# Kernel optimization log

Hardware: AMD Instinct MI355X
Metric: run time of the kernel (lower is better)

## Reference

```python
import jax, jax.numpy as jnp
import numpy as np
from jax import lax

V = 50000      # node_num
LN = 128       # feat_dim
S = 16         # stat_dim
E = 500000     # n_edges
T = 3          # propagation steps
MU = 0.9


def setup_inputs() -> dict:
    key = jax.random.key(0)
    ks = jax.random.split(key, 10)
    X_Node = jax.random.randint(ks[0], (E,), 0, V, dtype=jnp.int32)
    X_Neis = jax.random.randint(ks[1], (E,), 0, V, dtype=jnp.int32)
    dg_list = jax.random.randint(ks[2], (E,), 1, 64, dtype=jnp.int32)
    emb = jax.random.normal(ks[3], (V, LN), dtype=jnp.float32) * 0.1
    xi_w = jax.random.normal(ks[4], (2 * LN, S * S), dtype=jnp.float32) * (1.0 / np.sqrt(2 * LN))
    xi_b = jnp.zeros((S * S,), dtype=jnp.float32)
    rou_w = jax.random.normal(ks[5], (LN, S), dtype=jnp.float32) * (1.0 / np.sqrt(LN))
    rou_b = jnp.zeros((S,), dtype=jnp.float32)
    lin_w = jax.random.normal(ks[6], (LN + S, 3), dtype=jnp.float32) * (1.0 / np.sqrt(LN + S))
    lin_b = jnp.zeros((3,), dtype=jnp.float32)
    return {"X_Node": X_Node, "X_Neis": X_Neis, "dg_list": dg_list,
            "emb": emb, "xi_w": xi_w, "xi_b": xi_b,
            "rou_w": rou_w, "rou_b": rou_b, "lin_w": lin_w, "lin_b": lin_b}


def reference(X_Node, X_Neis, dg_list, emb, xi_w, xi_b, rou_w, rou_b, lin_w, lin_b):
    # edge features: concat(src embed, nbr embed) -> [E, 2*ln]
    Xn = emb[X_Node]                                  # [E, ln]
    X = jnp.concatenate([Xn, emb[X_Neis]], axis=1)    # [E, 2*ln]
    dg = dg_list.astype(emb.dtype)
    # Hw: A = Xi(X)*mu/s/dg  (constant across iterations; torch recomputes, same math)
    A = jnp.tanh(X @ xi_w + xi_b).reshape(-1, S, S)   # [E, s, s]
    A = A * (MU / S) / dg[:, None, None]
    b = jnp.tanh(Xn @ rou_w + rou_b)                  # [E, s]

    states0 = jnp.zeros((V, S), dtype=emb.dtype)

    def step(states, _):
        H = states[X_Node]                            # [E, s] gather
        H = jnp.einsum('est,et->es', A, H) + b        # per-edge small matvec
        states = jax.ops.segment_sum(H, X_Neis, num_segments=V)  # scatter-sum (AggrSum)
        return states, None

    states, _ = lax.scan(step, states0, None, length=T)
    logits = jnp.concatenate([emb, states], axis=1) @ lin_w + lin_b  # [V, 3]
    return jax.nn.softmax(logits, axis=1)
```

## Files before the change

### kernel.cpp

```cpp
#include <hip/hip_runtime.h>
#include <hip/hip_bf16.h>
#include <hip/hip_fp16.h>

#define LN_F 128

typedef __attribute__((ext_vector_type(8))) __bf16 bf16x8;
typedef __attribute__((ext_vector_type(4))) float f32x4;
typedef __attribute__((ext_vector_type(2))) _Float16 half2_t;

__device__ __forceinline__ unsigned short f2bf(float f) {
    unsigned u = __float_as_uint(f);
    u = u + 0x7FFFu + ((u >> 16) & 1u);
    return (unsigned short)(u >> 16);
}
__device__ __forceinline__ float tanh_polyc(float x) {
    x = fminf(1.2f, fmaxf(-1.2f, x));
    float t = x * x;
    float p = fmaf(t, -0.05396825397f, 0.13333333333f);
    p = fmaf(t, p, -0.33333333333f);
    p = fmaf(t, p, 1.0f);
    return x * p;
}
__device__ __forceinline__ float bflo(unsigned u) { return __uint_as_float(u << 16); }
__device__ __forceinline__ float bfhi(unsigned u) { return __uint_as_float(u & 0xffff0000u); }

__device__ __forceinline__ unsigned f2e5(float x) {
    unsigned short u = __half_as_ushort(__float2half(x));
    u = (unsigned short)(u + 0x7F + ((u >> 8) & 1));
    return (unsigned)(u >> 8) & 0xFFu;
}
__device__ __forceinline__ half2_t u2h2(unsigned w) {
    union { unsigned u; half2_t h; } c; c.u = w; return c.h;
}
__device__ __forceinline__ unsigned h2u(half2_t h) {
    union { half2_t h; unsigned u; } c; c.h = h; return c.u;
}
__device__ __forceinline__ half2_t tanh_pk(half2_t x) {
    const half2_t c2 = {(_Float16)(2.0f / 15.0f), (_Float16)(2.0f / 15.0f)};
    const half2_t c1 = {(_Float16)(-1.0f / 3.0f), (_Float16)(-1.0f / 3.0f)};
    const half2_t one = {(_Float16)1.0f, (_Float16)1.0f};
    half2_t t = x * x;
    half2_t p = t * c2 + c1;
    p = t * p + one;
    return x * p;
}

__global__ void k_conv(const float* __restrict__ emb, const float* __restrict__ xiw,
                       const float* __restrict__ rw,
                       unsigned short* __restrict__ embb, unsigned short* __restrict__ WcT,
                       unsigned short* __restrict__ rouT, int V) {
    int t = blockIdx.x * blockDim.x + threadIdx.x;
    int n_emb = V * 16;
    if (t < n_emb) {
        const float4* s = (const float4*)emb;
        float4 a = s[t * 2], b = s[t * 2 + 1];
        uint4 o;
        o.x = (unsigned)f2bf(a.x) | ((unsigned)f2bf(a.y) << 16);
        o.y = (unsigned)f2bf(a.z) | ((unsigned)f2bf(a.w) << 16);
        o.z = (unsigned)f2bf(b.x) | ((unsigned)f2bf(b.y) << 16);
        o.w = (unsigned)f2bf(b.z) | ((unsigned)f2bf(b.w) << 16);
        ((uint4*)embb)[t] = o;
    } else if (t < n_emb + 512 * 16) {
        int t2 = t - n_emb;
        int cp = t2 >> 4, g = t2 & 15;
        unsigned short u[8];
#pragma unroll
        for (int j = 0; j < 8; ++j) {
            int k = g * 8 + j;
            float w = (cp < 256) ? xiw[k * 256 + cp] : xiw[(128 + k) * 256 + (cp - 256)];
            u[j] = f2bf(w);
        }
        uint4 o;
        o.x = (unsigned)u[0] | ((unsigned)u[1] << 16);
        o.y = (unsigned)u[2] | ((unsigned)u[3] << 16);
        o.z = (unsigned)u[4] | ((unsigned)u[5] << 16);
        o.w = (unsigned)u[6] | ((unsigned)u[7] << 16);
        ((uint4*)WcT)[cp * 16 + (g ^ (cp & 7))] = o;
    } else if (t < n_emb + 512 * 16 + 256) {
        int t2 = t - n_emb - 512 * 16;
        int c = t2 >> 4, g = t2 & 15;
        unsigned short u[8];
#pragma unroll
        for (int j = 0; j < 8; ++j) u[j] = f2bf(rw[(g * 8 + j) * 16 + c]);
        uint4 o;
        o.x = (unsigned)u[0] | ((unsigned)u[1] << 16);
        o.y = (unsigned)u[2] | ((unsigned)u[3] << 16);
        o.z = (unsigned)u[4] | ((unsigned)u[5] << 16);
        o.w = (unsigned)u[6] | ((unsigned)u[7] << 16);
        ((uint4*)rouT)[c * 16 + (g ^ (c & 7))] = o;
    }
}

__global__ void k_hist(const int* __restrict__ Xe, int* __restrict__ cnt, int n) {
    int e = blockIdx.x * blockDim.x + threadIdx.x;
    if (e < n) atomicAdd(&cnt[Xe[e]], 1);
}

__global__ __launch_bounds__(256) void k_scan1(const int* __restrict__ cnt,
                                               int* __restrict__ rp,
                                               int* __restrict__ bsum, int V) {
    __shared__ int ls[256];
    int b = blockIdx.x, t = threadIdx.x;
    int i = b * 256 + t;
    int val = (i < V) ? cnt[i] : 0;
    ls[t] = val;
    __syncthreads();
    for (int off = 1; off < 256; off <<= 1) {
        int x = (t >= off) ? ls[t - off] : 0;
        __syncthreads();
        ls[t] += x;
        __syncthreads();
    }
    if (i < V) rp[i] = ls[t] - val;
    if (t == 255) bsum[b] = ls[255];
}

__global__ __launch_bounds__(256) void k_scan2(const int* __restrict__ bsum,
                                               int* __restrict__ boff,
                                               int* __restrict__ rp, int V, int NB) {
    __shared__ int ls[256];
    int t = threadIdx.x;
    int val = (t < NB) ? bsum[t] : 0;
    ls[t] = val;
    __syncthreads();
    for (int off = 1; off < 256; off <<= 1) {
        int x = (t >= off) ? ls[t - off] : 0;
        __syncthreads();
        ls[t] += x;
        __syncthreads();
    }
    if (t < NB) boff[t] = ls[t] - val;
    if (t == 255) rp[V] = ls[255];
}

__global__ void k_scan3(int* __restrict__ rp, const int* __restrict__ boff, int V) {
    int i = blockIdx.x * blockDim.x + threadIdx.x;
    if (i < V) rp[i] += boff[blockIdx.x];
}

__global__ void k_permute(const int* __restrict__ Xn, const int* __restrict__ Xe,
                          const int* __restrict__ dg, const int* __restrict__ rp,
                          int* __restrict__ c2, int2* __restrict__ edata,
                          int* __restrict__ edst, int n) {
    int e = blockIdx.x * blockDim.x + threadIdx.x;
    if (e >= n) return;
    int nb = Xe[e];
    int pos = rp[nb] + atomicAdd(&c2[nb], 1);
    edata[pos] = make_int2(Xn[e], __float_as_int(0.05625f / (float)dg[e]));
    edst[pos] = nb;
}

__global__ void k_padfill(int2* __restrict__ edata, int* __restrict__ edst,
                          int E, int Epad) {
    int i = E + blockIdx.x * blockDim.x + threadIdx.x;
    if (i >= Epad) return;
    edata[i] = make_int2(0, 0);
    edst[i] = 0;
}

__global__ __launch_bounds__(512) void k_U(
    const unsigned short* __restrict__ embb, const uint4* __restrict__ WcT,
    const uint4* __restrict__ rouT, const float* __restrict__ xib,
    const float* __restrict__ roub,
    unsigned* __restrict__ U8, unsigned* __restrict__ U28,
    float* __restrict__ bnode, int V) {
    __shared__ uint4 sB[2048];
    __shared__ uint4 sR[256];
    const int half = blockIdx.y;
    for (int i = threadIdx.x; i < 2048; i += 512) sB[i] = WcT[half * 2048 + i];
    if (half == 0 && threadIdx.x < 256) sR[threadIdx.x] = rouT[threadIdx.x];
    __syncthreads();

    const int wave = threadIdx.x >> 6, lane = threadIdx.x & 63;
    const int j = lane & 15, kg = lane >> 4;
    const int wbase = blockIdx.x * 512 + wave * 64;

    int nv[4];
#pragma unroll
    for (int g = 0; g < 4; ++g) nv[g] = min(wbase + g * 16 + j, V - 1);

    f32x4 acc[8][4] = {};
    f32x4 accb[4] = {};
#pragma unroll
    for (int kc = 0; kc < 4; ++kc) {
        bf16x8 bf[4];
#pragma unroll
        for (int g = 0; g < 4; ++g)
            bf[g] = *(const bf16x8*)(embb + (size_t)nv[g] * 128 + kc * 32 + kg * 8);
        int swz = (kc * 4 + kg) ^ (j & 7);
#pragma unroll
        for (int ct = 0; ct < 8; ++ct) {
            bf16x8 afr = ((const bf16x8*)sB)[(ct * 16 + j) * 16 + swz];
#pragma unroll
            for (int g = 0; g < 4; ++g)
                acc[ct][g] = __builtin_amdgcn_mfma_f32_16x16x32_bf16(afr, bf[g], acc[ct][g], 0, 0, 0);
        }
        if (half == 0) {
            bf16x8 rfr = ((const bf16x8*)sR)[j * 16 + swz];
#pragma unroll
            for (int g = 0; g < 4; ++g)
                accb[g] = __builtin_amdgcn_mfma_f32_16x16x32_bf16(rfr, bf[g], accb[g], 0, 0, 0);
        }
    }

#pragma unroll
    for (int ct = 0; ct < 8; ++ct) {
        int c0 = half * 128 + ct * 16 + kg * 4;
        float4 bias = (half < 2) ? ((const float4*)xib)[c0 >> 2]
                                 : make_float4(0.f, 0.f, 0.f, 0.f);
#pragma unroll
        for (int g = 0; g < 4; ++g) {
            int node = wbase + g * 16 + j;
            if (node < V) {
                const f32x4 a = acc[ct][g];
                float v0 = a[0] + bias.x, v1 = a[1] + bias.y;
                float v2 = a[2] + bias.z, v3 = a[3] + bias.w;
                unsigned pk = f2e5(v0) | (f2e5(v1) << 8) | (f2e5(v2) << 16) | (f2e5(v3) << 24);
                if (half < 2) U8[node * 64 + (c0 >> 2)] = pk;
                else          U28[node * 64 + ((c0 - 256) >> 2)] = pk;
            }
        }
    }
    if (half == 0) {
        float4 rb4 = ((const float4*)roub)[kg];
#pragma unroll
        for (int g = 0; g < 4; ++g) {
            int node = wbase + g * 16 + j;
            if (node < V) {
                float4 bo;
                bo.x = tanh_polyc(accb[g][0] + rb4.x);
                bo.y = tanh_polyc(accb[g][1] + rb4.y);
                bo.z = tanh_polyc(accb[g][2] + rb4.z);
                bo.w = tanh_polyc(accb[g][3] + rb4.w);
                *(float4*)(bnode + (size_t)node * 16 + kg * 4) = bo;
            }
        }
    }
}

__global__ __launch_bounds__(256) void k_B1e(
    const float* __restrict__ bnode, const int2* __restrict__ edata,
    const int* __restrict__ edst, float* __restrict__ B1, int E, int Epad) {
    int wid = (blockIdx.x * 256 + threadIdx.x) >> 6;
    int wbase = wid * 64;
    if (wbase >= Epad) return;
    int lane = threadIdx.x & 63;
    int g = lane >> 4, s = lane & 15, lbase = g * 16;
    int sbase = wbase + g * 16;

    int em = wbase + lane;
    int d_own = edst[em];
    int d_nxt = edst[min(em + 1, Epad - 1)];
    unsigned long long flags = __ballot(d_own != d_nxt);

    int cur = edst[sbase];
    float acc = 0.f;
#pragma unroll 4
    for (int j = 0; j < 16; ++j) {
        int p = sbase + j;
        int u = edata[p].x;
        float v = bnode[(size_t)u * 16 + s];
        acc += (p < E) ? v : 0.f;
        bool flush = ((flags >> (lbase + j)) & 1ull) || (j == 15);
        if (flush) {
            atomicAdd(&B1[(size_t)cur * 16 + s], acc);
            acc = 0.f;
            if (j < 15) cur = edst[p + 1];
        }
    }
}

__global__ void k_prep(const float* __restrict__ st, unsigned* __restrict__ Hf,
                       float* __restrict__ cp1, float* __restrict__ cp2, int n2) {
    int i = blockIdx.x * blockDim.x + threadIdx.x;
    if (i >= n2) return;
    float2 f = ((const float2*)st)[i];
    half2_t h = {(_Float16)f.x, (_Float16)f.y};
    Hf[i] = h2u(h);
    if (cp1 != nullptr) {
        ((float2*)cp1)[i] = f;
        ((float2*)cp2)[i] = f;
    }
}

__global__ __launch_bounds__(256) void k_prop_e(
    const unsigned* __restrict__ U8, const unsigned* __restrict__ U28,
    const int2* __restrict__ edata, const int* __restrict__ edst,
    const unsigned* __restrict__ Hf,
    float* __restrict__ sn, int Epad) {
    int wid = (blockIdx.x * 256 + threadIdx.x) >> 6;
    int wbase = wid * 64;
    if (wbase >= Epad) return;
    int lane = threadIdx.x & 63;
    int g = lane >> 4, s = lane & 15, lbase = g * 16;
    int sbase = wbase + g * 16;

    int em = wbase + lane;
    int d_own = edst[em];
    int d_nxt = edst[min(em + 1, Epad - 1)];
    unsigned long long flags = __ballot(d_own != d_nxt);

    int cur = edst[sbase];
    half2_t u2h[8];
    {
        uint4 r = ((const uint4*)U28)[cur * 16 + s];
        unsigned wr[4] = {r.x, r.y, r.z, r.w};
#pragma unroll
        for (int q = 0; q < 4; ++q) {
            u2h[2 * q]     = u2h2(__builtin_amdgcn_perm(wr[q], 0u, 0x05000400u));
            u2h[2 * q + 1] = u2h2(__builtin_amdgcn_perm(wr[q], 0u, 0x07000600u));
        }
    }

    float acc = 0.f;
#pragma unroll 2
    for (int j = 0; j < 16; ++j) {
        int p = sbase + j;
        int2 ed = edata[p];
        int u = ed.x;
        float sc = __int_as_float(ed.y);
        uint4 q1 = ((const uint4*)U8)[u * 16 + s];
        unsigned h2 = Hf[u * 8 + (s & 7)];
        unsigned wq[4] = {q1.x, q1.y, q1.z, q1.w};
        float sum = 0.f;
#pragma unroll
        for (int q = 0; q < 4; ++q) {
            half2_t x0 = u2h2(__builtin_amdgcn_perm(wq[q], 0u, 0x05000400u)) + u2h[2 * q];
            half2_t x1 = u2h2(__builtin_amdgcn_perm(wq[q], 0u, 0x07000600u)) + u2h[2 * q + 1];
            half2_t r0 = tanh_pk(x0);
            half2_t r1 = tanh_pk(x1);
            unsigned hm0 = __shfl(h2, lbase + 2 * q, 64);
            unsigned hm1 = __shfl(h2, lbase + 2 * q + 1, 64);
            sum = __builtin_amdgcn_fdot2(r0, u2h2(hm0), sum, false);
            sum = __builtin_amdgcn_fdot2(r1, u2h2(hm1), sum, false);
        }
        acc = fmaf(sc, sum, acc);
        bool flush = ((flags >> (lbase + j)) & 1ull) || (j == 15);
        if (flush) {
            atomicAdd(&sn[(size_t)cur * 16 + s], acc);
            acc = 0.f;
            if (j < 15) {
                cur = edst[p + 1];
                uint4 r = ((const uint4*)U28)[cur * 16 + s];
                unsigned wr[4] = {r.x, r.y, r.z, r.w};
#pragma unroll
                for (int q = 0; q < 4; ++q) {
                    u2h[2 * q]     = u2h2(__builtin_amdgcn_perm(wr[q], 0u, 0x05000400u));
                    u2h[2 * q + 1] = u2h2(__builtin_amdgcn_perm(wr[q], 0u, 0x07000600u));
                }
            }
        }
    }
}

__global__ void k_final(const unsigned short* __restrict__ embb, const float* __restrict__ st,
                        const float* __restrict__ lw, const float* __restrict__ lb,
                        float* __restrict__ out, int nv) {
    __shared__ float sw[435];
    for (int i = threadIdx.x; i < 435; i += 256) sw[i] = (i < 432) ? lw[i] : lb[i - 432];
    __syncthreads();
    int t = blockIdx.x * blockDim.x + threadIdx.x;
    int v = t >> 4, j = t & 15;
    if (v >= nv) return;
    const uint4 q = *(const uint4*)(embb + (size_t)v * 128 + j * 8);
    unsigned uu[4] = {q.x, q.y, q.z, q.w};
    float a0 = 0.f, a1 = 0.f, a2 = 0.f;
#pragma unroll
    for (int m = 0; m < 4; ++m) {
        int i = j * 8 + 2 * m;
        float x0 = bflo(uu[m]), x1 = bfhi(uu[m]);
        a0 += x0 * sw[i * 3] + x1 * sw[(i + 1) * 3];
        a1 += x0 * sw[i * 3 + 1] + x1 * sw[(i + 1) * 3 + 1];
        a2 += x0 * sw[i * 3 + 2] + x1 * sw[(i + 1) * 3 + 2];
    }
    float xs = st[(size_t)v * 16 + j];
    a0 += xs * sw[(128 + j) * 3]; a1 += xs * sw[(128 + j) * 3 + 1]; a2 += xs * sw[(128 + j) * 3 + 2];
#pragma unroll
    for (int m = 1; m < 16; m <<= 1) {
        a0 += __shfl_xor(a0, m, 64);
        a1 += __shfl_xor(a1, m, 64);
        a2 += __shfl_xor(a2, m, 64);
    }
    if (j == 0) {
        a0 += sw[432]; a1 += sw[433]; a2 += sw[434];
        float mx = fmaxf(a0, fmaxf(a1, a2));
        float e0 = __expf(a0 - mx), e1 = __expf(a1 - mx), e2 = __expf(a2 - mx);
        float inv = 1.f / (e0 + e1 + e2);
        out[(size_t)v * 3 + 0] = e0 * inv;
        out[(size_t)v * 3 + 1] = e1 * inv;
        out[(size_t)v * 3 + 2] = e2 * inv;
    }
}

extern "C" void kernel_launch(void* const* d_in, const int* in_sizes, int n_in,
                              void* d_out, int out_size, void* d_ws, size_t ws_size,
                              hipStream_t stream) {
    const int*   Xn  = (const int*)d_in[0];
    const int*   Xe  = (const int*)d_in[1];
    const int*   dg  = (const int*)d_in[2];
    const float* emb = (const float*)d_in[3];
    const float* xiw = (const float*)d_in[4];
    const float* xib = (const float*)d_in[5];
    const float* rw  = (const float*)d_in[6];
    const float* rb  = (const float*)d_in[7];
    const float* lw  = (const float*)d_in[8];
    const float* lb  = (const float*)d_in[9];
    float* out = (float*)d_out;
    const int E = in_sizes[0];
    const int V = in_sizes[3] / LN_F;
    const int NB = (V + 255) / 256;
    const int Epad = (E + 63) & ~63;

    char* p = (char*)d_ws;
    auto carve = [&](size_t bytes) {
        char* q = p; p += (bytes + 255) & ~(size_t)255; return q;
    };
    unsigned short* embb = (unsigned short*)carve((size_t)V * 128 * 2);
    unsigned* U8    = (unsigned*)carve((size_t)V * 256);
    unsigned* U28   = (unsigned*)carve((size_t)V * 256);
    uint4* WcT   = (uint4*)carve(512 * 16 * 16);
    uint4* rouT  = (uint4*)carve(4096);
    float* bnode = (float*)carve((size_t)V * 16 * 4);
    float* B1    = (float*)carve((size_t)V * 16 * 4);
    float* stB   = (float*)carve((size_t)V * 16 * 4);
    float* stA   = (float*)carve((size_t)V * 16 * 4);
    unsigned* Hf = (unsigned*)carve((size_t)V * 16 * 2);
    int*   cnt   = (int*)carve((size_t)V * 4 * 2);
    int*   c2    = cnt + V;
    int*   rp    = (int*)carve((size_t)(V + 1) * 4);
    int*   bsum  = (int*)carve(256 * 4);
    int*   boff  = (int*)carve(256 * 4);
    int2*  edata = (int2*)carve((size_t)Epad * 8);
    int*   edst  = (int*)carve((size_t)Epad * 4);

    {
        int nconv = V * 16 + 512 * 16 + 256;
        k_conv<<<(nconv + 255) / 256, 256, 0, stream>>>(
            emb, xiw, rw, embb, (unsigned short*)WcT, (unsigned short*)rouT, V);
        dim3 g((V + 511) / 512, 4);
        k_U<<<g, 512, 0, stream>>>(embb, WcT, rouT, xib, rb, U8, U28, bnode, V);
    }

    hipMemsetAsync(cnt, 0, (size_t)V * 4 * 2, stream);
    k_hist<<<(E + 255) / 256, 256, 0, stream>>>(Xe, cnt, E);
    k_scan1<<<NB, 256, 0, stream>>>(cnt, rp, bsum, V);
    k_scan2<<<1, 256, 0, stream>>>(bsum, boff, rp, V, NB);
    k_scan3<<<NB, 256, 0, stream>>>(rp, boff, V);
    k_permute<<<(E + 255) / 256, 256, 0, stream>>>(Xn, Xe, dg, rp, c2, edata, edst, E);
    if (Epad > E)
        k_padfill<<<1, 64, 0, stream>>>(edata, edst, E, Epad);

    hipMemsetAsync(B1, 0, (size_t)V * 16 * 4, stream);
    {
        int blocks = (Epad / 64 + 3) / 4;
        k_B1e<<<blocks, 256, 0, stream>>>(bnode, edata, edst, B1, E, Epad);
    }

    const int n2 = V * 8;
    const int pblocks = (Epad / 64 + 3) / 4;

    k_prep<<<(n2 + 255) / 256, 256, 0, stream>>>(B1, Hf, stB, stA, n2);
    k_prop_e<<<pblocks, 256, 0, stream>>>(U8, U28, edata, edst, Hf, stB, Epad);

    k_prep<<<(n2 + 255) / 256, 256, 0, stream>>>(stB, Hf, nullptr, nullptr, n2);
    k_prop_e<<<pblocks, 256, 0, stream>>>(U8, U28, edata, edst, Hf, stA, Epad);

    k_final<<<((size_t)V * 16 + 255) / 256, 256, 0, stream>>>(embb, stA, lw, lb, out, V);
}
```

Measured before the change: 201.8 us.

## Fuse histogram and B1 zeroing into conversion kernel; shuffle edge data across lanes

Merges the destination histogram and the B1 zero-fill into the bf16 conversion kernel, folds the pad fill into the permute kernel, and zeroes both counter arrays with a single memset. This cuts kernel launches and memsets. In the edge kernels, each lane now loads its own edata and edst entry once, and the inner loops read them with wave shuffles instead of repeated global loads. The unroll factor of the propagation loop rises from 2 to 4. The extra shuffles add instruction overhead, and the larger unroll may raise register pressure.

```diff
diff --git a/kernel.cpp b/kernel.cpp
--- a/kernel.cpp
+++ b/kernel.cpp
@@ -46,9 +46,10 @@
 }
 
 __global__ void k_conv(const float* __restrict__ emb, const float* __restrict__ xiw,
-                       const float* __restrict__ rw,
+                       const float* __restrict__ rw, const int* __restrict__ Xe,
                        unsigned short* __restrict__ embb, unsigned short* __restrict__ WcT,
-                       unsigned short* __restrict__ rouT, int V) {
+                       unsigned short* __restrict__ rouT, int* __restrict__ cnt,
+                       float* __restrict__ B1, int V, int E) {
     int t = blockIdx.x * blockDim.x + threadIdx.x;
     int n_emb = V * 16;
     if (t < n_emb) {
@@ -60,6 +61,7 @@
         o.z = (unsigned)f2bf(b.x) | ((unsigned)f2bf(b.y) << 16);
         o.w = (unsigned)f2bf(b.z) | ((unsigned)f2bf(b.w) << 16);
         ((uint4*)embb)[t] = o;
+        B1[t] = 0.f;
     } else if (t < n_emb + 512 * 16) {
         int t2 = t - n_emb;
         int cp = t2 >> 4, g = t2 & 15;
@@ -89,11 +91,7 @@
         o.w = (unsigned)u[6] | ((unsigned)u[7] << 16);
         ((uint4*)rouT)[c * 16 + (g ^ (c & 7))] = o;
     }
-}
-
-__global__ void k_hist(const int* __restrict__ Xe, int* __restrict__ cnt, int n) {
-    int e = blockIdx.x * blockDim.x + threadIdx.x;
-    if (e < n) atomicAdd(&cnt[Xe[e]], 1);
+    if (t < E) atomicAdd(&cnt[Xe[t]], 1);
 }
 
 __global__ __launch_bounds__(256) void k_scan1(const int* __restrict__ cnt,
@@ -141,21 +139,17 @@
 __global__ void k_permute(const int* __restrict__ Xn, const int* __restrict__ Xe,
                           const int* __restrict__ dg, const int* __restrict__ rp,
                           int* __restrict__ c2, int2* __restrict__ edata,
-                          int* __restrict__ edst, int n) {
+                          int* __restrict__ edst, int n, int Epad) {
     int e = blockIdx.x * blockDim.x + threadIdx.x;
-    if (e >= n) return;
-    int nb = Xe[e];
-    int pos = rp[nb] + atomicAdd(&c2[nb], 1);
-    edata[pos] = make_int2(Xn[e], __float_as_int(0.05625f / (float)dg[e]));
-    edst[pos] = nb;
-}
-
-__global__ void k_padfill(int2* __restrict__ edata, int* __restrict__ edst,
-                          int E, int Epad) {
-    int i = E + blockIdx.x * blockDim.x + threadIdx.x;
-    if (i >= Epad) return;
-    edata[i] = make_int2(0, 0);
-    edst[i] = 0;
+    if (e < n) {
+        int nb = Xe[e];
+        int pos = rp[nb] + atomicAdd(&c2[nb], 1);
+        edata[pos] = make_int2(Xn[e], __float_as_int(0.05625f / (float)dg[e]));
+        edst[pos] = nb;
+    } else if (e < Epad) {
+        edata[e] = make_int2(0, 0);
+        edst[e] = 0;
+    }
 }
 
 __global__ __launch_bounds__(512) void k_U(
@@ -246,26 +240,27 @@
     if (wbase >= Epad) return;
     int lane = threadIdx.x & 63;
     int g = lane >> 4, s = lane & 15, lbase = g * 16;
-    int sbase = wbase + g * 16;
+    int sbase = wbase + lbase;
 
     int em = wbase + lane;
+    int my_u = edata[em].x;
     int d_own = edst[em];
     int d_nxt = edst[min(em + 1, Epad - 1)];
     unsigned long long flags = __ballot(d_own != d_nxt);
 
-    int cur = edst[sbase];
+    int cur = __shfl(d_own, lbase, 64);
     float acc = 0.f;
 #pragma unroll 4
     for (int j = 0; j < 16; ++j) {
         int p = sbase + j;
-        int u = edata[p].x;
+        int u = __shfl(my_u, lbase + j, 64);
         float v = bnode[(size_t)u * 16 + s];
         acc += (p < E) ? v : 0.f;
         bool flush = ((flags >> (lbase + j)) & 1ull) || (j == 15);
         if (flush) {
             atomicAdd(&B1[(size_t)cur * 16 + s], acc);
             acc = 0.f;
-            if (j < 15) cur = edst[p + 1];
+            if (j < 15) cur = __shfl(d_nxt, lbase + j, 64);
         }
     }
 }
@@ -293,14 +288,14 @@
     if (wbase >= Epad) return;
     int lane = threadIdx.x & 63;
     int g = lane >> 4, s = lane & 15, lbase = g * 16;
-    int sbase = wbase + g * 16;
 
     int em = wbase + lane;
+    int2 myed = edata[em];
     int d_own = edst[em];
     int d_nxt = edst[min(em + 1, Epad - 1)];
     unsigned long long flags = __ballot(d_own != d_nxt);
 
-    int cur = edst[sbase];
+    int cur = __shfl(d_own, lbase, 64);
     half2_t u2h[8];
     {
         uint4 r = ((const uint4*)U28)[cur * 16 + s];
@@ -313,12 +308,10 @@
     }
 
     float acc = 0.f;
-#pragma unroll 2
+#pragma unroll 4
     for (int j = 0; j < 16; ++j) {
-        int p = sbase + j;
-        int2 ed = edata[p];
-        int u = ed.x;
-        float sc = __int_as_float(ed.y);
+        int u = __shfl(myed.x, lbase + j, 64);
+        float sc = __int_as_float(__shfl(myed.y, lbase + j, 64));
         uint4 q1 = ((const uint4*)U8)[u * 16 + s];
         unsigned h2 = Hf[u * 8 + (s & 7)];
         unsigned wq[4] = {q1.x, q1.y, q1.z, q1.w};
@@ -340,7 +333,7 @@
             atomicAdd(&sn[(size_t)cur * 16 + s], acc);
             acc = 0.f;
             if (j < 15) {
-                cur = edst[p + 1];
+                cur = __shfl(d_nxt, lbase + j, 64);
                 uint4 r = ((const uint4*)U28)[cur * 16 + s];
                 unsigned wr[4] = {r.x, r.y, r.z, r.w};
 #pragma unroll
@@ -415,50 +408,54 @@
     auto carve = [&](size_t bytes) {
         char* q = p; p += (bytes + 255) & ~(size_t)255; return q;
     };
+    int*   cnt   = (int*)carve((size_t)V * 4);
+    int*   c2    = (int*)carve((size_t)V * 4);
+    size_t zero_bytes = (size_t)(p - (char*)cnt);
+    float* B1    = (float*)carve((size_t)V * 16 * 4);
     unsigned short* embb = (unsigned short*)carve((size_t)V * 128 * 2);
     unsigned* U8    = (unsigned*)carve((size_t)V * 256);
     unsigned* U28   = (unsigned*)carve((size_t)V * 256);
     uint4* WcT   = (uint4*)carve(512 * 16 * 16);
     uint4* rouT  = (uint4*)carve(4096);
     float* bnode = (float*)carve((size_t)V * 16 * 4);
-    float* B1    = (float*)carve((size_t)V * 16 * 4);
     float* stB   = (float*)carve((size_t)V * 16 * 4);
     float* stA   = (float*)carve((size_t)V * 16 * 4);
     unsigned* Hf = (unsigned*)carve((size_t)V * 16 * 2);
-    int*   cnt   = (int*)carve((size_t)V * 4 * 2);
-    int*   c2    = cnt + V;
     int*   rp    = (int*)carve((size_t)(V + 1) * 4);
     int*   bsum  = (int*)carve(256 * 4);
     int*   boff  = (int*)carve(256 * 4);
     int2*  edata = (int2*)carve((size_t)Epad * 8);
     int*   edst  = (int*)carve((size_t)Epad * 4);
 
+    hipMemsetAsync(cnt, 0, zero_bytes, stream);
+
     {
         int nconv = V * 16 + 512 * 16 + 256;
-        k_conv<<<(nconv + 255) / 256, 256, 0, stream>>>(
-            emb, xiw, rw, embb, (unsigned short*)WcT, (unsigned short*)rouT, V);
-        dim3 g((V + 511) / 512, 4);
-        k_U<<<g, 512, 0, stream>>>(embb, WcT, rouT, xib, rb, U8, U28, bnode, V);
-    }
-
-    hipMemsetAsync(cnt, 0, (size_t)V * 4 * 2, stream);
-    k_hist<<<(E + 255) / 256, 256, 0, stream>>>(Xe, cnt, E);
+        int ntot = nconv > E ? nconv : E;
+        k_conv<<<(ntot + 255) / 256, 256, 0, stream>>>(
+            emb, xiw, rw, Xe, embb, (unsigned short*)WcT, (unsigned short*)rouT,
+            cnt, B1, V, E);
+    }
+
     k_scan1<<<NB, 256, 0, stream>>>(cnt, rp, bsum, V);
     k_scan2<<<1, 256, 0, stream>>>(bsum, boff, rp, V, NB);
     k_scan3<<<NB, 256, 0, stream>>>(rp, boff, V);
-    k_permute<<<(E + 255) / 256, 256, 0, stream>>>(Xn, Xe, dg, rp, c2, edata, edst, E);
-    if (Epad > E)
-        k_padfill<<<1, 64, 0, stream>>>(edata, edst, E, Epad);
-
-    hipMemsetAsync(B1, 0, (size_t)V * 16 * 4, stream);
+
     {
-        int blocks = (Epad / 64 + 3) / 4;
-        k_B1e<<<blocks, 256, 0, stream>>>(bnode, edata, edst, B1, E, Epad);
+        int ng = (Epad > E ? Epad : E);
+        k_permute<<<(ng + 255) / 256, 256, 0, stream>>>(Xn, Xe, dg, rp, c2, edata, edst, E, Epad);
+    }
+
+    {
+        dim3 g((V + 511) / 512, 4);
+        k_U<<<g, 512, 0, stream>>>(embb, WcT, rouT, xib, rb, U8, U28, bnode, V);
     }
 
     const int n2 = V * 8;
     const int pblocks = (Epad / 64 + 3) / 4;
 
+    k_B1e<<<pblocks, 256, 0, stream>>>(bnode, edata, edst, B1, E, Epad);
+
     k_prep<<<(n2 + 255) / 256, 256, 0, stream>>>(B1, Hf, stB, stA, n2);
     k_prop_e<<<pblocks, 256, 0, stream>>>(U8, U28, edata, edst, Hf, stB, Epad);
 
```

New measurement: 184.6 us. 8.5% less time.
